# Kernel optimization log

Hardware: AMD Instinct MI355X
Metric: run time of the kernel (lower is better)

## Reference

```python
import jax, jax.numpy as jnp
import numpy as np

N = 8192       # nodes
E = 262144     # edges (avg degree 32)
F_IN, H, L = 512, 256, 64


def setup_inputs() -> dict:
    key = jax.random.key(0)
    ks = jax.random.split(key, 8)
    features = jax.random.normal(ks[0], (N, F_IN), dtype=jnp.float32)
    src = jax.random.randint(ks[1], (E,), 0, N)
    dst = jax.random.randint(ks[2], (E,), 0, N)
    # nn.Linear weights are [out_feats, in_feats]; scale ~ kaiming-ish small init
    W1 = jax.random.normal(ks[3], (H, F_IN), dtype=jnp.float32) * (1.0 / np.sqrt(F_IN))
    b1 = jnp.zeros((H,), dtype=jnp.float32)
    W2 = jax.random.normal(ks[4], (L, H), dtype=jnp.float32) * (1.0 / np.sqrt(H))
    b2 = jnp.zeros((L,), dtype=jnp.float32)
    W3 = jax.random.normal(ks[5], (L, H), dtype=jnp.float32) * (1.0 / np.sqrt(H))
    b3 = jnp.zeros((L,), dtype=jnp.float32)
    return {"features": features, "src": src, "dst": dst,
            "W1": W1, "b1": b1, "W2": W2, "b2": b2, "W3": W3, "b3": b3}


def _gcn_agg(h, src, dst):
    # DGL copy_src + sum: gather source node features along edges, scatter-sum to dst
    return jax.ops.segment_sum(h[src], dst, num_segments=N)  # [N, d]


def reference(features, src, dst, W1, b1, W2, b2, W3, b3):
    # GCN layer 1: aggregate then linear + relu  (dropout=0 -> identity)
    agg1 = _gcn_agg(features, src, dst)                 # [N, F_IN]
    hidden = jax.nn.relu(agg1 @ W1.T + b1)              # [N, H]
    # GCN layers 2 & 3 share the aggregated hidden (linear activation)
    agg2 = _gcn_agg(hidden, src, dst)                   # [N, H]
    mu = agg2 @ W2.T + b2                               # [N, L]
    logvar = agg2 @ W3.T + b3                           # [N, L]
    # eval-mode reparameterize: z = mu
    z = mu
    # inner-product decoder with sigmoid
    adj = jax.nn.sigmoid(z @ z.T)                       # [N, N]
    return adj, mu, logvar
```

## Files before the change

kernel.cpp:

```cpp
#include <hip/hip_runtime.h>
#include <hip/hip_bf16.h>

#define N_NODES 8192
#define N_EDGES 262144

typedef __attribute__((ext_vector_type(8))) short short8v;
typedef __attribute__((ext_vector_type(4))) float float4v;

static __device__ __forceinline__ unsigned short f2bf(float f) {
    unsigned u = __float_as_uint(f);
    unsigned r = (u + 0x7FFF + ((u >> 16) & 1)) >> 16;
    return (unsigned short)r;
}
static __device__ __forceinline__ float bf2f(unsigned short h) {
    return __uint_as_float(((unsigned)h) << 16);
}


__global__ __launch_bounds__(256) void hist_prep_kernel(const int* __restrict__ dst, int* __restrict__ deg,
                                                        const float* __restrict__ X, const float* __restrict__ W1,
                                                        const float* __restrict__ W2, const float* __restrict__ W3,
                                                        unsigned short* __restrict__ Xb,
                                                        unsigned short* __restrict__ W1b,
                                                        unsigned short* __restrict__ W23b) {
    int b = blockIdx.x;
    if (b < 1024) {
        int e = b * 256 + threadIdx.x;
        atomicAdd(&deg[dst[e]], 1);
        return;
    }
    int i4 = ((b - 1024) * 256 + threadIdx.x) * 4;
    const float* srcp;
    unsigned short* dstp;
    int off;
    if (i4 < 4194304)      { srcp = X;  dstp = Xb;           off = i4; }
    else if (i4 < 4325376) { srcp = W1; dstp = W1b;          off = i4 - 4194304; }
    else if (i4 < 4341760) { srcp = W2; dstp = W23b;         off = i4 - 4325376; }
    else                   { srcp = W3; dstp = W23b + 16384; off = i4 - 4341760; }
    float4 v = *(const float4*)&srcp[off];
    ushort4 o = {f2bf(v.x), f2bf(v.y), f2bf(v.z), f2bf(v.w)};
    *(ushort4*)&dstp[off] = o;
}


__global__ __launch_bounds__(1024) void scan_kernel(const int* __restrict__ deg, int* __restrict__ offs,
                                                    int* __restrict__ cur) {
    __shared__ int sums[1024];
    int t = threadIdx.x;
    int v[8];
    int s = 0;
#pragma unroll
    for (int i = 0; i < 8; i++) { v[i] = deg[t * 8 + i]; s += v[i]; }
    sums[t] = s;
    __syncthreads();
    for (int off = 1; off < 1024; off <<= 1) {
        int x = (t >= off) ? sums[t - off] : 0;
        __syncthreads();
        sums[t] += x;
        __syncthreads();
    }
    int ex = (t == 0) ? 0 : sums[t - 1];
#pragma unroll
    for (int i = 0; i < 8; i++) { offs[t * 8 + i] = ex; cur[t * 8 + i] = ex; ex += v[i]; }
    if (t == 1023) offs[N_NODES] = ex;
}

__global__ __launch_bounds__(256) void scatter_kernel(const int* __restrict__ src, const int* __restrict__ dst,
                                                      int* __restrict__ cur, int* __restrict__ csr) {
    int e = blockIdx.x * 256 + threadIdx.x;
    int d = dst[e];
    int p = atomicAdd(&cur[d], 1);
    csr[p] = src[e];
}


template <int MI, int NJ, int WN>
__global__ __launch_bounds__(256) void gemm_nt_mfma(const unsigned short* __restrict__ A,
                                                    const unsigned short* __restrict__ B,
                                                    unsigned short* __restrict__ C,
                                                    int N, int K) {
    constexpr int MW = 4 / WN;
    const int tid = threadIdx.x;
    const int lane = tid & 63;
    const int w = tid >> 6;
    const int r = lane & 15, q = lane >> 4;
    const int m0 = blockIdx.x * (MI * 16 * MW) + (w / WN) * (MI * 16);
    const int n0 = blockIdx.y * (NJ * 16 * WN) + (w % WN) * (NJ * 16);
    const unsigned short* Ap = &A[q * 8];
    const unsigned short* Bp = &B[q * 8];
    float4v acc[MI][NJ] = {};
    short8v a[MI], b[NJ], an[MI], bn[NJ];
#pragma unroll
    for (int i = 0; i < MI; i++) a[i] = *(const short8v*)&Ap[(size_t)(m0 + i * 16 + r) * K];
#pragma unroll
    for (int j = 0; j < NJ; j++) b[j] = *(const short8v*)&Bp[(size_t)(n0 + j * 16 + r) * K];
    for (int k = 32; k < K; k += 32) {
#pragma unroll
        for (int i = 0; i < MI; i++) an[i] = *(const short8v*)&Ap[(size_t)(m0 + i * 16 + r) * K + k];
#pragma unroll
        for (int j = 0; j < NJ; j++) bn[j] = *(const short8v*)&Bp[(size_t)(n0 + j * 16 + r) * K + k];
#pragma unroll
        for (int i = 0; i < MI; i++)
#pragma unroll
            for (int j = 0; j < NJ; j++)
                acc[i][j] = __builtin_amdgcn_mfma_f32_16x16x32_bf16(a[i], b[j], acc[i][j], 0, 0, 0);
#pragma unroll
        for (int i = 0; i < MI; i++) a[i] = an[i];
#pragma unroll
        for (int j = 0; j < NJ; j++) b[j] = bn[j];
    }
#pragma unroll
    for (int i = 0; i < MI; i++)
#pragma unroll
        for (int j = 0; j < NJ; j++)
            acc[i][j] = __builtin_amdgcn_mfma_f32_16x16x32_bf16(a[i], b[j], acc[i][j], 0, 0, 0);
#pragma unroll
    for (int i = 0; i < MI; i++)
#pragma unroll
        for (int j = 0; j < NJ; j++) {
            int col = n0 + j * 16 + r;
#pragma unroll
            for (int t = 0; t < 4; t++) {
                int row = m0 + i * 16 + q * 4 + t;
                C[(size_t)row * N + col] = f2bf(acc[i][j][t]);
            }
        }
}


__global__ __launch_bounds__(256) void agg_relu_kernel(const unsigned short* __restrict__ Yb,
                                                       const int* __restrict__ offs,
                                                       const int* __restrict__ csr, const float* __restrict__ bias,
                                                       unsigned short* __restrict__ out) {
    int node = blockIdx.x * 4 + (threadIdx.x >> 6);
    int lane = threadIdx.x & 63;
    int s = offs[node], e = offs[node + 1];
    float4 acc0 = {0.f, 0.f, 0.f, 0.f}, acc1 = {0.f, 0.f, 0.f, 0.f};
    int i = s;
    for (; i + 3 < e; i += 4) {
        int u0 = csr[i], u1 = csr[i + 1], u2 = csr[i + 2], u3 = csr[i + 3];
        ushort4 v0 = *(const ushort4*)&Yb[(size_t)u0 * 256 + lane * 4];
        ushort4 v1 = *(const ushort4*)&Yb[(size_t)u1 * 256 + lane * 4];
        ushort4 v2 = *(const ushort4*)&Yb[(size_t)u2 * 256 + lane * 4];
        ushort4 v3 = *(const ushort4*)&Yb[(size_t)u3 * 256 + lane * 4];
        acc0.x += bf2f(v0.x) + bf2f(v1.x); acc1.x += bf2f(v2.x) + bf2f(v3.x);
        acc0.y += bf2f(v0.y) + bf2f(v1.y); acc1.y += bf2f(v2.y) + bf2f(v3.y);
        acc0.z += bf2f(v0.z) + bf2f(v1.z); acc1.z += bf2f(v2.z) + bf2f(v3.z);
        acc0.w += bf2f(v0.w) + bf2f(v1.w); acc1.w += bf2f(v2.w) + bf2f(v3.w);
    }
    for (; i < e; i++) {
        int u = csr[i];
        ushort4 v = *(const ushort4*)&Yb[(size_t)u * 256 + lane * 4];
        acc0.x += bf2f(v.x); acc0.y += bf2f(v.y); acc0.z += bf2f(v.z); acc0.w += bf2f(v.w);
    }
    float4 b = *(const float4*)&bias[lane * 4];
    ushort4 o;
    o.x = f2bf(fmaxf(acc0.x + acc1.x + b.x, 0.f));
    o.y = f2bf(fmaxf(acc0.y + acc1.y + b.y, 0.f));
    o.z = f2bf(fmaxf(acc0.z + acc1.z + b.z, 0.f));
    o.w = f2bf(fmaxf(acc0.w + acc1.w + b.w, 0.f));
    *(ushort4*)&out[(size_t)node * 256 + lane * 4] = o;
}


__global__ __launch_bounds__(256) void agg_split_kernel(const unsigned short* __restrict__ Zb,
                                                        const int* __restrict__ offs,
                                                        const int* __restrict__ csr, const float* __restrict__ b2,
                                                        const float* __restrict__ b3, float* __restrict__ mu,
                                                        float* __restrict__ lv, unsigned short* __restrict__ zb) {
    int node = blockIdx.x * 4 + (threadIdx.x >> 6);
    int lane = threadIdx.x & 63;
    int s = offs[node], e = offs[node + 1];
    float2 acc0 = {0.f, 0.f}, acc1 = {0.f, 0.f};
    int i = s;
    for (; i + 3 < e; i += 4) {
        int u0 = csr[i], u1 = csr[i + 1], u2 = csr[i + 2], u3 = csr[i + 3];
        ushort2 v0 = *(const ushort2*)&Zb[(size_t)u0 * 128 + lane * 2];
        ushort2 v1 = *(const ushort2*)&Zb[(size_t)u1 * 128 + lane * 2];
        ushort2 v2 = *(const ushort2*)&Zb[(size_t)u2 * 128 + lane * 2];
        ushort2 v3 = *(const ushort2*)&Zb[(size_t)u3 * 128 + lane * 2];
        acc0.x += bf2f(v0.x) + bf2f(v1.x); acc1.x += bf2f(v2.x) + bf2f(v3.x);
        acc0.y += bf2f(v0.y) + bf2f(v1.y); acc1.y += bf2f(v2.y) + bf2f(v3.y);
    }
    for (; i < e; i++) {
        int u = csr[i];
        ushort2 v = *(const ushort2*)&Zb[(size_t)u * 128 + lane * 2];
        acc0.x += bf2f(v.x); acc0.y += bf2f(v.y);
    }
    float2 acc = {acc0.x + acc1.x, acc0.y + acc1.y};
    int col = lane * 2;
    if (col < 64) {
        acc.x += b2[col]; acc.y += b2[col + 1];
        *(float2*)&mu[(size_t)node * 64 + col] = acc;
        ushort2 q = {f2bf(acc.x), f2bf(acc.y)};
        *(ushort2*)&zb[(size_t)node * 64 + col] = q;
    } else {
        col -= 64;
        acc.x += b3[col]; acc.y += b3[col + 1];
        *(float2*)&lv[(size_t)node * 64 + col] = acc;
    }
}


__global__ __launch_bounds__(256) void adj_mfma_kernel(const unsigned short* __restrict__ zb,
                                                       float* __restrict__ out) {
    const int tid = threadIdx.x;
    const int lane = tid & 63;
    const int wid = tid >> 6;
    const int waveM = wid >> 1, waveN = wid & 1;
    const int m_base = blockIdx.x * 128 + waveM * 64;
    const int n_base = blockIdx.y * 128 + waveN * 64;
    const int r = lane & 15;
    const int q = lane >> 4;

    short8v a[4][2], b[4][2];
#pragma unroll
    for (int i = 0; i < 4; i++)
#pragma unroll
        for (int s = 0; s < 2; s++) {
            a[i][s] = *(const short8v*)&zb[(size_t)(m_base + i * 16 + r) * 64 + s * 32 + q * 8];
            b[i][s] = *(const short8v*)&zb[(size_t)(n_base + i * 16 + r) * 64 + s * 32 + q * 8];
        }

    float4v acc[4][4] = {};
#pragma unroll
    for (int s = 0; s < 2; s++)
#pragma unroll
        for (int i = 0; i < 4; i++)
#pragma unroll
            for (int j = 0; j < 4; j++)
                acc[i][j] = __builtin_amdgcn_mfma_f32_16x16x32_bf16(a[i][s], b[j][s], acc[i][j], 0, 0, 0);

#pragma unroll
    for (int i = 0; i < 4; i++)
#pragma unroll
        for (int j = 0; j < 4; j++) {
            int col = n_base + j * 16 + r;
#pragma unroll
            for (int t = 0; t < 4; t++) {
                int row = m_base + i * 16 + q * 4 + t;
                float v = 1.0f / (1.0f + __expf(-acc[i][j][t]));
                out[(size_t)row * N_NODES + col] = v;
            }
        }
}


extern "C" void kernel_launch(void* const* d_in, const int* in_sizes, int n_in,
                              void* d_out, int out_size, void* d_ws, size_t ws_size,
                              hipStream_t stream) {
    const float* X   = (const float*)d_in[0];
    const int*   src = (const int*)d_in[1];
    const int*   dst = (const int*)d_in[2];
    const float* W1  = (const float*)d_in[3];
    const float* b1  = (const float*)d_in[4];
    const float* W2  = (const float*)d_in[5];
    const float* b2  = (const float*)d_in[6];
    const float* W3  = (const float*)d_in[7];
    const float* b3  = (const float*)d_in[8];

    float* out    = (float*)d_out;
    float* adj    = out;
    float* mu_out = out + (size_t)N_NODES * N_NODES;
    float* lv_out = mu_out + (size_t)N_NODES * 64;

    char* ws = (char*)d_ws;
    size_t off = 0;
    auto alloc = [&](size_t bytes) -> void* {
        void* p = ws + off;
        off += (bytes + 1023) & ~(size_t)1023;
        return p;
    };
    int* deg            = (int*)alloc(N_NODES * 4);
    int* cur            = (int*)alloc(N_NODES * 4);
    int* offs           = (int*)alloc((N_NODES + 1) * 4);
    int* csr            = (int*)alloc(N_EDGES * 4);
    unsigned short* Xb  = (unsigned short*)alloc((size_t)N_NODES * 512 * 2);
    unsigned short* W1b = (unsigned short*)alloc(256 * 512 * 2);
    unsigned short* W23b= (unsigned short*)alloc(128 * 256 * 2);
    unsigned short* Y1b = (unsigned short*)alloc((size_t)N_NODES * 256 * 2);
    unsigned short* Hb  = (unsigned short*)alloc((size_t)N_NODES * 256 * 2);
    unsigned short* Zb  = (unsigned short*)alloc((size_t)N_NODES * 128 * 2);
    unsigned short* zb  = (unsigned short*)alloc((size_t)N_NODES * 64 * 2);

    hipMemsetAsync(deg, 0, N_NODES * sizeof(int), stream);
    hist_prep_kernel<<<5280, 256, 0, stream>>>(dst, deg, X, W1, W2, W3, Xb, W1b, W23b);
    scan_kernel<<<1, 1024, 0, stream>>>(deg, offs, cur);
    scatter_kernel<<<N_EDGES / 256, 256, 0, stream>>>(src, dst, cur, csr);

    gemm_nt_mfma<2, 2, 4><<<dim3(256, 2), 256, 0, stream>>>(Xb, W1b, Y1b, 256, 512);
    agg_relu_kernel<<<N_NODES / 4, 256, 0, stream>>>(Y1b, offs, csr, b1, Hb);
    gemm_nt_mfma<2, 1, 4><<<dim3(256, 2), 256, 0, stream>>>(Hb, W23b, Zb, 128, 256);
    agg_split_kernel<<<N_NODES / 4, 256, 0, stream>>>(Zb, offs, csr, b2, b3, mu_out, lv_out, zb);
    adj_mfma_kernel<<<dim3(64, 64), 256, 0, stream>>>(zb, adj);
}
```

Before: 376.2 us.

## Fuse CSR scatter with first GEMM launch and use warp-shuffle scan

Merges the edge scatter kernel and the first bf16 MFMA GEMM into one launch, where the first 1024 blocks do the scatter and the remaining 512 blocks do the GEMM. The two are independent, so they can overlap and one launch is saved. Separately, the single-block prefix scan swaps its shared-memory Hillis-Steele loop, which needed many barriers, for 64-lane shuffle scans plus a 16-entry cross-wave pass. Running the scatter's atomics alongside the GEMM in one grid may change block scheduling and contention.

```diff
diff --git a/kernel.cpp b/kernel.cpp
--- a/kernel.cpp
+++ b/kernel.cpp
@@ -45,47 +45,51 @@
 
 __global__ __launch_bounds__(1024) void scan_kernel(const int* __restrict__ deg, int* __restrict__ offs,
                                                     int* __restrict__ cur) {
-    __shared__ int sums[1024];
+    __shared__ int wsum[16];
     int t = threadIdx.x;
+    int lane = t & 63, w = t >> 6;
     int v[8];
     int s = 0;
 #pragma unroll
     for (int i = 0; i < 8; i++) { v[i] = deg[t * 8 + i]; s += v[i]; }
-    sums[t] = s;
+    int x = s;
+#pragma unroll
+    for (int off = 1; off < 64; off <<= 1) {
+        int y = __shfl_up(x, off, 64);
+        if (lane >= off) x += y;
+    }
+    if (lane == 63) wsum[w] = x;
     __syncthreads();
-    for (int off = 1; off < 1024; off <<= 1) {
-        int x = (t >= off) ? sums[t - off] : 0;
-        __syncthreads();
-        sums[t] += x;
-        __syncthreads();
-    }
-    int ex = (t == 0) ? 0 : sums[t - 1];
+    if (w == 0 && lane < 16) {
+        int ws = wsum[lane];
+        int xx = ws;
+#pragma unroll
+        for (int off2 = 1; off2 < 16; off2 <<= 1) {
+            int yy = __shfl_up(xx, off2, 64);
+            if (lane >= off2) xx += yy;
+        }
+        wsum[lane] = xx - ws;
+    }
+    __syncthreads();
+    int ex = wsum[w] + (x - s);
 #pragma unroll
     for (int i = 0; i < 8; i++) { offs[t * 8 + i] = ex; cur[t * 8 + i] = ex; ex += v[i]; }
     if (t == 1023) offs[N_NODES] = ex;
 }
 
-__global__ __launch_bounds__(256) void scatter_kernel(const int* __restrict__ src, const int* __restrict__ dst,
-                                                      int* __restrict__ cur, int* __restrict__ csr) {
-    int e = blockIdx.x * 256 + threadIdx.x;
-    int d = dst[e];
-    int p = atomicAdd(&cur[d], 1);
-    csr[p] = src[e];
-}
-
 
 template <int MI, int NJ, int WN>
-__global__ __launch_bounds__(256) void gemm_nt_mfma(const unsigned short* __restrict__ A,
-                                                    const unsigned short* __restrict__ B,
-                                                    unsigned short* __restrict__ C,
-                                                    int N, int K) {
+__device__ __forceinline__ void gemm_nt_body(const unsigned short* __restrict__ A,
+                                             const unsigned short* __restrict__ B,
+                                             unsigned short* __restrict__ C,
+                                             int N, int K, int bx, int by) {
     constexpr int MW = 4 / WN;
     const int tid = threadIdx.x;
     const int lane = tid & 63;
     const int w = tid >> 6;
     const int r = lane & 15, q = lane >> 4;
-    const int m0 = blockIdx.x * (MI * 16 * MW) + (w / WN) * (MI * 16);
-    const int n0 = blockIdx.y * (NJ * 16 * WN) + (w % WN) * (NJ * 16);
+    const int m0 = bx * (MI * 16 * MW) + (w / WN) * (MI * 16);
+    const int n0 = by * (NJ * 16 * WN) + (w % WN) * (NJ * 16);
     const unsigned short* Ap = &A[q * 8];
     const unsigned short* Bp = &B[q * 8];
     float4v acc[MI][NJ] = {};
@@ -125,6 +129,31 @@
                 C[(size_t)row * N + col] = f2bf(acc[i][j][t]);
             }
         }
+}
+
+
+__global__ __launch_bounds__(256) void scatter_gemm1_kernel(const int* __restrict__ src,
+                                                            const int* __restrict__ dst,
+                                                            int* __restrict__ cur, int* __restrict__ csr,
+                                                            const unsigned short* __restrict__ A,
+                                                            const unsigned short* __restrict__ B,
+                                                            unsigned short* __restrict__ C) {
+    int b = blockIdx.x;
+    if (b < 1024) {
+        int e = b * 256 + threadIdx.x;
+        int d = dst[e];
+        int p = atomicAdd(&cur[d], 1);
+        csr[p] = src[e];
+        return;
+    }
+    int id = b - 1024;
+    gemm_nt_body<2, 2, 4>(A, B, C, 256, 512, id & 255, id >> 8);
+}
+
+__global__ __launch_bounds__(256) void gemm2_kernel(const unsigned short* __restrict__ A,
+                                                    const unsigned short* __restrict__ B,
+                                                    unsigned short* __restrict__ C) {
+    gemm_nt_body<2, 1, 4>(A, B, C, 128, 256, blockIdx.x, blockIdx.y);
 }
 
 
@@ -286,11 +315,9 @@
     hipMemsetAsync(deg, 0, N_NODES * sizeof(int), stream);
     hist_prep_kernel<<<5280, 256, 0, stream>>>(dst, deg, X, W1, W2, W3, Xb, W1b, W23b);
     scan_kernel<<<1, 1024, 0, stream>>>(deg, offs, cur);
-    scatter_kernel<<<N_EDGES / 256, 256, 0, stream>>>(src, dst, cur, csr);
-
-    gemm_nt_mfma<2, 2, 4><<<dim3(256, 2), 256, 0, stream>>>(Xb, W1b, Y1b, 256, 512);
+    scatter_gemm1_kernel<<<1536, 256, 0, stream>>>(src, dst, cur, csr, Xb, W1b, Y1b);
     agg_relu_kernel<<<N_NODES / 4, 256, 0, stream>>>(Y1b, offs, csr, b1, Hb);
-    gemm_nt_mfma<2, 1, 4><<<dim3(256, 2), 256, 0, stream>>>(Hb, W23b, Zb, 128, 256);
+    gemm2_kernel<<<dim3(256, 2), 256, 0, stream>>>(Hb, W23b, Zb);
     agg_split_kernel<<<N_NODES / 4, 256, 0, stream>>>(Zb, offs, csr, b2, b3, mu_out, lv_out, zb);
     adj_mfma_kernel<<<dim3(64, 64), 256, 0, stream>>>(zb, adj);
 }
```

Result: slower. 386.2 us (+2.7%).
